# Optimization experiments

Hardware: AMD Instinct MI355X
Metric: run time of the kernel (lower is better)

## Reference

```python
import jax, jax.numpy as jnp
import numpy as np

C, H, OUT = 64, 128, 64          # in_channels, hidden_dim, out_channels
N, E = 20000, 640000             # nodes, edges
LN_EPS = 1e-5


def layer_norm(x, g, b):
    mu = jnp.mean(x, axis=-1, keepdims=True)
    var = jnp.var(x, axis=-1, keepdims=True)
    return (x - mu) * jax.lax.rsqrt(var + LN_EPS) * g + b


def setup_inputs() -> dict:
    key = jax.random.key(0)
    ks = jax.random.split(key, 12)
    F = 2 * C + 5  # edge MLP input dim = 133

    def w(k, shape, fan_in):
        return jax.random.normal(k, shape, jnp.float32) / np.float32(np.sqrt(fan_in))

    return {
        "x": jax.random.normal(ks[0], (N, C), jnp.float32),
        "pos": jax.random.normal(ks[1], (N, 2), jnp.float32),
        "vel": jax.random.normal(ks[2], (N, 2), jnp.float32),
        # phi_e: Linear(F,H) -> LN -> Softplus -> Linear(H,H) -> Softplus -> Linear(H,H)
        "We1": w(ks[3], (F, H), F), "be1": jnp.zeros((H,), jnp.float32),
        "ge1": jnp.ones((H,), jnp.float32), "bte1": jnp.zeros((H,), jnp.float32),
        "We2": w(ks[4], (H, H), H), "be2": jnp.zeros((H,), jnp.float32),
        "We3": w(ks[5], (H, H), H), "be3": jnp.zeros((H,), jnp.float32),
        # phi_v: Linear(F,H) -> LN -> Softplus -> Linear(H,1)
        "Wv1": w(ks[6], (F, H), F), "bv1": jnp.zeros((H,), jnp.float32),
        "gv1": jnp.ones((H,), jnp.float32), "btv1": jnp.zeros((H,), jnp.float32),
        "Wv2": w(ks[7], (H, 1), H), "bv2": jnp.zeros((1,), jnp.float32),
        # phi_h: Linear(C+H+1,H) -> LN -> Softplus -> Linear(H,OUT)
        "Wh1": w(ks[8], (C + H + 1, H), C + H + 1), "bh1": jnp.zeros((H,), jnp.float32),
        "gh1": jnp.ones((H,), jnp.float32), "bth1": jnp.zeros((H,), jnp.float32),
        "Wh2": w(ks[9], (H, OUT), H), "bh2": jnp.zeros((OUT,), jnp.float32),
        "edge_index": jax.random.randint(ks[10], (2, E), 0, N, dtype=jnp.int64)
        if jax.config.jax_enable_x64 else jax.random.randint(ks[10], (2, E), 0, N, dtype=jnp.int32),
    }


def reference(x, pos, vel,
              We1, be1, ge1, bte1, We2, be2, We3, be3,
              Wv1, bv1, gv1, btv1, Wv2, bv2,
              Wh1, bh1, gh1, bth1, Wh2, bh2,
              edge_index):
    src = edge_index[0]  # j (source / x_j)
    dst = edge_index[1]  # i (target / x_i, aggregation index)

    # per-edge geometric features (gather)
    rel_pos = pos[src] - pos[dst]                                   # [E,2]
    rel_vel = vel[src] - vel[dst]                                   # [E,2]
    dist_sq = jnp.sum(rel_pos ** 2, axis=-1, keepdims=True)         # [E,1]
    dot_vr = jnp.sum(rel_vel * rel_pos, axis=-1, keepdims=True)     # [E,1]
    r2_inv = jnp.minimum(1.0 / (dist_sq + 0.05), 20.0)
    r6_inv = jnp.minimum(r2_inv ** 3, 400.0)
    r12_inv = jnp.minimum(r6_inv ** 2, 160000.0)

    tmp = jnp.concatenate([x[dst], x[src], dist_sq, dot_vr,
                           r2_inv, r6_inv, r12_inv], axis=1)        # [E, 2C+5]

    # phi_e (edge MLP)
    h = jax.nn.softplus(layer_norm(tmp @ We1 + be1, ge1, bte1))
    h = jax.nn.softplus(h @ We2 + be2)
    m_h_e = h @ We3 + be3                                           # [E,H]

    # phi_v (scalar weight on rel_pos -> equivariant vector message)
    v = jax.nn.softplus(layer_norm(tmp @ Wv1 + bv1, gv1, btv1))
    v_w = v @ Wv2 + bv2                                             # [E,1]
    m_v_e = v_w * rel_pos                                           # [E,2]

    # scatter-mean aggregation to target nodes
    n_nodes = x.shape[0]
    ones = jnp.ones((src.shape[0], 1), x.dtype)
    cnt = jax.ops.segment_sum(ones, dst, num_segments=n_nodes)
    denom = jnp.maximum(cnt, 1.0)
    m_h = jax.ops.segment_sum(m_h_e, dst, num_segments=n_nodes) / denom   # [N,H]
    m_v = jax.ops.segment_sum(m_v_e, dst, num_segments=n_nodes) / denom   # [N,2]

    m_v_norm = jnp.sqrt(jnp.sum((m_v + 1e-8) ** 2, axis=-1, keepdims=True))  # [N,1]

    # phi_h (node update MLP); shortcut is Identity since C == OUT
    hin = jnp.concatenate([x, m_h, m_v_norm], axis=-1)              # [N, C+H+1]
    hu = jax.nn.softplus(layer_norm(hin @ Wh1 + bh1, gh1, bth1))
    h_update = hu @ Wh2 + bh2                                       # [N,OUT]
    return x + h_update
```

## Files before the change

### kernel.cpp

```cpp
#include <hip/hip_runtime.h>
#include <stdint.h>

#define NCH    64
#define HID    128
#define OUTC   64
#define NNODE  20000
#define NEDGE  640000
#define FDIM   133
#define TE     32
#define TN     32
#define LN_EPS 1e-5f
#define KP1    160
#define KP2    128
#define KN1    224
#define CAGS   130
#define NEBLK  (NEDGE / TE)
#define XSTR   (NEBLK / 8)

typedef __attribute__((ext_vector_type(8))) short bf16x8;
typedef __attribute__((ext_vector_type(4))) float f32x4;

__device__ __forceinline__ unsigned short f2bf(float f) {
    union { float f; unsigned int i; } v; v.f = f;
    unsigned int b = v.i;
    return (unsigned short)((b + 0x7FFFu + ((b >> 16) & 1u)) >> 16);
}
#if defined(__has_builtin)
#if __has_builtin(__builtin_amdgcn_cvt_pk_bf16_f32)
#define HAVE_PK_BF16 1
#endif
#endif
__device__ __forceinline__ unsigned int f2bf_pk(float a, float b) {
#ifdef HAVE_PK_BF16
    auto r = __builtin_amdgcn_cvt_pk_bf16_f32(a, b);
    return __builtin_bit_cast(unsigned int, r);
#else
    return (unsigned int)f2bf(a) | ((unsigned int)f2bf(b) << 16);
#endif
}
__device__ __forceinline__ float bfu2f(unsigned short u) {
    union { unsigned int i; float f; } v; v.i = ((unsigned int)u) << 16; return v.f;
}
__device__ __forceinline__ float sp(float xv) {
    return fmaxf(xv, 0.f) + __logf(1.0f + __expf(-fabsf(xv)));
}
__device__ __forceinline__ void atomAddF(float* p, float v) {
    __hip_atomic_fetch_add(p, v, __ATOMIC_RELAXED, __HIP_MEMORY_SCOPE_AGENT);
}
template<int PAT> __device__ __forceinline__ float shx(float v) {
    int i = __builtin_amdgcn_ds_swizzle(__builtin_bit_cast(int, v), PAT);
    return __builtin_bit_cast(float, i);
}
#define RED16(v) { v += shx<0x041F>(v); v += shx<0x081F>(v); v += shx<0x101F>(v); v += shx<0x201F>(v); }

__device__ __forceinline__ int fragOff(int ks, int mt, int lanepos) {
    return ((ks * 2 + mt) * 64 + lanepos) * 8;
}

#define WT_WE1 0
#define WT_WV1 (128 * KP1)
#define WT_WE2 (2 * 128 * KP1)
#define WT_WE3 (2 * 128 * KP1 + 128 * KP2)
#define WT_WH1 (2 * 128 * KP1 + 2 * 128 * KP2)
#define WT_WH2 (WT_WH1 + 128 * KN1)
#define WT_TOTAL (WT_WH2 + 64 * KP2)
#define PKP_N  1153

__global__ __launch_bounds__(256)
void eg_prep(const float* __restrict__ We1, const float* __restrict__ Wv1,
             const float* __restrict__ We2, const float* __restrict__ We3,
             const float* __restrict__ Wh1, const float* __restrict__ Wh2,
             const float* __restrict__ be1, const float* __restrict__ bv1,
             const float* __restrict__ ge1, const float* __restrict__ bte1,
             const float* __restrict__ gv1, const float* __restrict__ btv1,
             const float* __restrict__ Wv2, const float* __restrict__ be2,
             const float* __restrict__ be3, const float* __restrict__ bv2,
             const int* __restrict__ ei,
             short* __restrict__ wt, float* __restrict__ pkp,
             int* __restrict__ deg)
{
    int idx = blockIdx.x * 256 + threadIdx.x;
    if (idx < WT_TOTAL) {
        short v;
        if (idx < WT_WV1) {
            int n = idx / KP1, k = idx % KP1;
            v = (k < FDIM) ? (short)f2bf(We1[(size_t)k * HID + n]) : (short)0;
        } else if (idx < WT_WE2) {
            int r = idx - WT_WV1; int n = r / KP1, k = r % KP1;
            v = (k < FDIM) ? (short)f2bf(Wv1[(size_t)k * HID + n]) : (short)0;
        } else if (idx < WT_WE3) {
            int r = idx - WT_WE2; int n = r / KP2, k = r % KP2;
            v = (short)f2bf(We2[(size_t)k * HID + n]);
        } else if (idx < WT_WH1) {
            int r = idx - WT_WE3; int n = r / KP2, k = r % KP2;
            v = (short)f2bf(We3[(size_t)k * HID + n]);
        } else if (idx < WT_WH2) {
            int r = idx - WT_WH1; int n = r / KN1, k = r % KN1;
            v = (k < 193) ? (short)f2bf(Wh1[(size_t)k * HID + n]) : (short)0;
        } else {
            int r = idx - WT_WH2; int n = r / KP2, k = r % KP2;
            v = (short)f2bf(Wh2[(size_t)k * OUTC + n]);
        }
        wt[idx] = v;
    }
    if (idx < PKP_N) {
        float pv;
        int k = idx >> 7, c = idx & 127;
        switch (k) {
            case 0: pv = be1[c]; break;
            case 1: pv = bv1[c]; break;
            case 2: pv = ge1[c]; break;
            case 3: pv = bte1[c]; break;
            case 4: pv = gv1[c]; break;
            case 5: pv = btv1[c]; break;
            case 6: pv = Wv2[c]; break;
            case 7: pv = be2[c]; break;
            case 8: pv = be3[c]; break;
            default: pv = bv2[0]; break;
        }
        pkp[idx] = pv;
    }
    if (idx < NEDGE)
        __hip_atomic_fetch_add(&deg[ei[NEDGE + idx]], 1, __ATOMIC_RELAXED, __HIP_MEMORY_SCOPE_AGENT);
}

__global__ __launch_bounds__(1024)
void eg_scan(const int* __restrict__ deg, int* __restrict__ cur)
{
    __shared__ int part[1024];
    const int tid = threadIdx.x;
    const int chunk = (NNODE + 1023) / 1024;
    const int base = tid * chunk;
    const int lim = min(base + chunk, NNODE);
    int s = 0;
    for (int j = base; j < lim; ++j) s += deg[j];
    part[tid] = s;
    __syncthreads();
    for (int off = 1; off < 1024; off <<= 1) {
        int v = (tid >= off) ? part[tid - off] : 0;
        __syncthreads();
        part[tid] += v;
        __syncthreads();
    }
    int run = (tid > 0) ? part[tid - 1] : 0;
    for (int j = base; j < lim; ++j) { cur[j] = run; run += deg[j]; }
}

__global__ __launch_bounds__(256)
void eg_scatter(const int* __restrict__ ei, int* __restrict__ cur,
                int* __restrict__ perm)
{
    int i = blockIdx.x * 256 + threadIdx.x;
    if (i < NEDGE) {
        int d = ei[NEDGE + i];
        int p = __hip_atomic_fetch_add(&cur[d], 1, __ATOMIC_RELAXED, __HIP_MEMORY_SCOPE_AGENT);
        perm[p] = i;
    }
}

__global__ __launch_bounds__(256, 7)
void eg_edge(const float* __restrict__ x, const float* __restrict__ pos,
             const float* __restrict__ vel,
             const float* __restrict__ pkp,
             const short* __restrict__ wt,
             const int* __restrict__ ei, const int* __restrict__ perm,
             float* __restrict__ mh, float* __restrict__ mv)
{
    __shared__ __align__(16) short frag_s[5 * 2 * 64 * 8];
    __shared__ __align__(4) unsigned short cagg_s[TE * CAGS];
    __shared__ float psum_s[512];
    __shared__ float mu_s[64], rs_s[64];
    __shared__ int   dst_s[TE], src_s[TE];
    __shared__ float rel_s[TE * 2], vw_s[TE];

    const int tid  = threadIdx.x;
    const int lane = tid & 63;
    const int wid  = tid >> 6;
    const int lr   = lane & 15;
    const int quad = lane >> 4;
    const int n0w  = wid * 32;
    const int bid  = (blockIdx.x & 7) * XSTR + (blockIdx.x >> 3);
    const int e_base = bid * TE;

    const short* We1T = wt + WT_WE1;
    const short* Wv1T = wt + WT_WV1;
    const short* We2T = wt + WT_WE2;
    const short* We3T = wt + WT_WE3;

    float geo[5];
    if (tid < TE) {
        int gi = perm[e_base + tid];
        int eS = ei[gi];
        int eD = ei[NEDGE + gi];
        src_s[tid] = eS; dst_s[tid] = eD;
        float rx = pos[2 * eS]     - pos[2 * eD];
        float ry = pos[2 * eS + 1] - pos[2 * eD + 1];
        float vx = vel[2 * eS]     - vel[2 * eD];
        float vy = vel[2 * eS + 1] - vel[2 * eD + 1];
        float dsq = rx * rx + ry * ry;
        float dvr = vx * rx + vy * ry;
        float r2  = fminf(1.0f / (dsq + 0.05f), 20.0f);
        float r6  = fminf(r2 * r2 * r2, 400.0f);
        float r12 = fminf(r6 * r6, 160000.0f);
        geo[0] = dsq; geo[1] = dvr; geo[2] = r2; geo[3] = r6; geo[4] = r12;
        rel_s[2 * tid] = rx; rel_s[2 * tid + 1] = ry;
    }
    if (tid < 128) {
        int4 z = {0, 0, 0, 0};
        *(int4*)&frag_s[4 * 2 * 64 * 8 + tid * 8] = z;
    }
    __syncthreads();

    if (tid < TE) {
        int off = fragOff(4, tid >> 4, (tid & 15));
        #pragma unroll
        for (int j = 0; j < 5; ++j) frag_s[off + j] = (short)f2bf(geo[j]);
    }
    {
        const int e = tid & 31, slot = tid >> 5;
        const int d = dst_s[e], s = src_s[e];
        #pragma unroll
        for (int h = 0; h < 2; ++h) {
            int o = slot + h * 8;
            int node = h ? s : d;
            int c0 = (o & 7) * 8;
            const float4 a0 = *(const float4*)&x[(size_t)node * NCH + c0];
            const float4 a1 = *(const float4*)&x[(size_t)node * NCH + c0 + 4];
            uint4 pk;
            pk.x = f2bf_pk(a0.x, a0.y); pk.y = f2bf_pk(a0.z, a0.w);
            pk.z = f2bf_pk(a1.x, a1.y); pk.w = f2bf_pk(a1.z, a1.w);
            int ks = o >> 2, kq = o & 3;
            *(uint4*)&frag_s[fragOff(ks, e >> 4, kq * 16 + (e & 15))] = pk;
        }
    }
    __syncthreads();

    const int ncol0 = n0w + lr;
    const int ncol1 = n0w + 16 + lr;
    const float* p0 = pkp + ncol0;
    const float* p1 = pkp + ncol1;

    f32x4 zero4 = {0.f, 0.f, 0.f, 0.f};
    f32x4 accE[2][2], accV[2][2];
    #pragma unroll
    for (int mt = 0; mt < 2; ++mt)
        #pragma unroll
        for (int nt = 0; nt < 2; ++nt) { accE[mt][nt] = zero4; accV[mt][nt] = zero4; }
    {
        const short* pa = &frag_s[lane * 8];
        const short* pwE0 = We1T + ncol0 * KP1 + quad * 8;
        const short* pwE1 = We1T + ncol1 * KP1 + quad * 8;
        const short* pwV0 = Wv1T + ncol0 * KP1 + quad * 8;
        const short* pwV1 = Wv1T + ncol1 * KP1 + quad * 8;
        #pragma unroll
        for (int ks = 0; ks < 5; ++ks) {
            bf16x8 af0 = *(const bf16x8*)&pa[ks * 1024];
            bf16x8 af1 = *(const bf16x8*)&pa[ks * 1024 + 512];
            bf16x8 bwE0 = *(const bf16x8*)&pwE0[ks * 32];
            bf16x8 bwE1 = *(const bf16x8*)&pwE1[ks * 32];
            bf16x8 bwV0 = *(const bf16x8*)&pwV0[ks * 32];
            bf16x8 bwV1 = *(const bf16x8*)&pwV1[ks * 32];
            accE[0][0] = __builtin_amdgcn_mfma_f32_16x16x32_bf16(af0, bwE0, accE[0][0], 0, 0, 0);
            accE[1][0] = __builtin_amdgcn_mfma_f32_16x16x32_bf16(af1, bwE0, accE[1][0], 0, 0, 0);
            accE[0][1] = __builtin_amdgcn_mfma_f32_16x16x32_bf16(af0, bwE1, accE[0][1], 0, 0, 0);
            accE[1][1] = __builtin_amdgcn_mfma_f32_16x16x32_bf16(af1, bwE1, accE[1][1], 0, 0, 0);
            accV[0][0] = __builtin_amdgcn_mfma_f32_16x16x32_bf16(af0, bwV0, accV[0][0], 0, 0, 0);
            accV[1][0] = __builtin_amdgcn_mfma_f32_16x16x32_bf16(af1, bwV0, accV[1][0], 0, 0, 0);
            accV[0][1] = __builtin_amdgcn_mfma_f32_16x16x32_bf16(af0, bwV1, accV[0][1], 0, 0, 0);
            accV[1][1] = __builtin_amdgcn_mfma_f32_16x16x32_bf16(af1, bwV1, accV[1][1], 0, 0, 0);
        }
    }
    {
        float be0 = p0[0], be_1 = p1[0];
        float bv0 = p0[128], bv_1 = p1[128];
        #pragma unroll
        for (int mt = 0; mt < 2; ++mt)
            #pragma unroll
            for (int r = 0; r < 4; ++r) {
                accE[mt][0][r] += be0; accE[mt][1][r] += be_1;
                accV[mt][0][r] += bv0; accV[mt][1][r] += bv_1;
            }
    }

    #pragma unroll
    for (int mt = 0; mt < 2; ++mt)
        #pragma unroll
        for (int r = 0; r < 4; ++r) {
            float se = accE[mt][0][r] + accE[mt][1][r];
            float qe = accE[mt][0][r] * accE[mt][0][r] + accE[mt][1][r] * accE[mt][1][r];
            float sv = accV[mt][0][r] + accV[mt][1][r];
            float qv = accV[mt][0][r] * accV[mt][0][r] + accV[mt][1][r] * accV[mt][1][r];
            RED16(se); RED16(qe); RED16(sv); RED16(qv);
            if (lr == 0) {
                int row = mt * 16 + quad * 4 + r;
                psum_s[      row * 4 + wid] = se;
                psum_s[128 + row * 4 + wid] = qe;
                psum_s[256 + row * 4 + wid] = sv;
                psum_s[384 + row * 4 + wid] = qv;
            }
        }
    __syncthreads();
    if (tid < 64) {
        int p = tid >> 5, row = tid & 31;
        float s = 0.f, q = 0.f;
        #pragma unroll
        for (int w = 0; w < 4; ++w) {
            s += psum_s[p * 256 +       row * 4 + w];
            q += psum_s[p * 256 + 128 + row * 4 + w];
        }
        float mu = s * (1.0f / HID);
        float var = q * (1.0f / HID) - mu * mu;
        mu_s[p * 32 + row] = mu;
        rs_s[p * 32 + row] = rsqrtf(var + LN_EPS);
    }
    __syncthreads();

    {
        float gE0 = p0[256], gE1 = p1[256];
        float tE0 = p0[384], tE1 = p1[384];
        float gV0 = p0[512], gV1 = p1[512];
        float tV0 = p0[640], tV1 = p1[640];
        float w20 = p0[768], w21 = p1[768];
        int ks0 = ncol0 >> 5, kq0 = (ncol0 & 31) >> 3, j0 = ncol0 & 7;
        int ks1 = ncol1 >> 5, kq1 = (ncol1 & 31) >> 3, j1 = ncol1 & 7;
        short* bp0 = &frag_s[(ks0 * 128 + kq0 * 16 + quad * 4) * 8 + j0];
        short* bp1 = &frag_s[(ks1 * 128 + kq1 * 16 + quad * 4) * 8 + j1];
        #pragma unroll
        for (int mt = 0; mt < 2; ++mt)
            #pragma unroll
            for (int r = 0; r < 4; ++r) {
                int rlow = quad * 4 + r, row = mt * 16 + rlow;
                float mu = mu_s[row], rsv = rs_s[row];
                float muV = mu_s[32 + row], rsV = rs_s[32 + row];
                float h0 = sp((accE[mt][0][r] - mu) * rsv * gE0 + tE0);
                float h1 = sp((accE[mt][1][r] - mu) * rsv * gE1 + tE1);
                unsigned int ph = f2bf_pk(h0, h1);
                bp0[mt * 512 + r * 8] = (short)(ph & 0xFFFFu);
                bp1[mt * 512 + r * 8] = (short)(ph >> 16);
                float v0 = sp((accV[mt][0][r] - muV) * rsV * gV0 + tV0);
                float v1 = sp((accV[mt][1][r] - muV) * rsV * gV1 + tV1);
                float vp = v0 * w20 + v1 * w21;
                RED16(vp);
                if (lr == 0) psum_s[row * 4 + wid] = vp;
            }
    }
    __syncthreads();
    if (tid < TE) {
        float s = 0.f;
        #pragma unroll
        for (int w = 0; w < 4; ++w) s += psum_s[tid * 4 + w];
        vw_s[tid] = s + pkp[1152];
    }

    {
        f32x4 acc2[2][2];
        #pragma unroll
        for (int mt = 0; mt < 2; ++mt)
            #pragma unroll
            for (int nt = 0; nt < 2; ++nt) acc2[mt][nt] = zero4;
        {
            const short* pa = &frag_s[lane * 8];
            const short* pw0 = We2T + ncol0 * KP2 + quad * 8;
            const short* pw1 = We2T + ncol1 * KP2 + quad * 8;
            #pragma unroll
            for (int ks = 0; ks < 4; ++ks) {
                bf16x8 af0 = *(const bf16x8*)&pa[ks * 1024];
                bf16x8 af1 = *(const bf16x8*)&pa[ks * 1024 + 512];
                bf16x8 bw0 = *(const bf16x8*)&pw0[ks * 32];
                bf16x8 bw1 = *(const bf16x8*)&pw1[ks * 32];
                acc2[0][0] = __builtin_amdgcn_mfma_f32_16x16x32_bf16(af0, bw0, acc2[0][0], 0, 0, 0);
                acc2[1][0] = __builtin_amdgcn_mfma_f32_16x16x32_bf16(af1, bw0, acc2[1][0], 0, 0, 0);
                acc2[0][1] = __builtin_amdgcn_mfma_f32_16x16x32_bf16(af0, bw1, acc2[0][1], 0, 0, 0);
                acc2[1][1] = __builtin_amdgcn_mfma_f32_16x16x32_bf16(af1, bw1, acc2[1][1], 0, 0, 0);
            }
        }
        __syncthreads();
        float b2a = p0[896], b2b = p1[896];
        int ksA = ncol0 >> 5, kqA = (ncol0 & 31) >> 3, jA = ncol0 & 7;
        int ksB = ncol1 >> 5, kqB = (ncol1 & 31) >> 3, jB = ncol1 & 7;
        short* bpA = &frag_s[(ksA * 128 + kqA * 16 + quad * 4) * 8 + jA];
        short* bpB = &frag_s[(ksB * 128 + kqB * 16 + quad * 4) * 8 + jB];
        #pragma unroll
        for (int mt = 0; mt < 2; ++mt)
            #pragma unroll
            for (int r = 0; r < 4; ++r) {
                bpA[mt * 512 + r * 8] = (short)f2bf(sp(acc2[mt][0][r] + b2a));
                bpB[mt * 512 + r * 8] = (short)f2bf(sp(acc2[mt][1][r] + b2b));
            }
    }
    __syncthreads();

    {
        f32x4 acc3[2][2];
        #pragma unroll
        for (int mt = 0; mt < 2; ++mt)
            #pragma unroll
            for (int nt = 0; nt < 2; ++nt) acc3[mt][nt] = zero4;
        {
            const short* pa = &frag_s[lane * 8];
            const short* pw0 = We3T + ncol0 * KP2 + quad * 8;
            const short* pw1 = We3T + ncol1 * KP2 + quad * 8;
            #pragma unroll
            for (int ks = 0; ks < 4; ++ks) {
                bf16x8 af0 = *(const bf16x8*)&pa[ks * 1024];
                bf16x8 af1 = *(const bf16x8*)&pa[ks * 1024 + 512];
                bf16x8 bw0 = *(const bf16x8*)&pw0[ks * 32];
                bf16x8 bw1 = *(const bf16x8*)&pw1[ks * 32];
                acc3[0][0] = __builtin_amdgcn_mfma_f32_16x16x32_bf16(af0, bw0, acc3[0][0], 0, 0, 0);
                acc3[1][0] = __builtin_amdgcn_mfma_f32_16x16x32_bf16(af1, bw0, acc3[1][0], 0, 0, 0);
                acc3[0][1] = __builtin_amdgcn_mfma_f32_16x16x32_bf16(af0, bw1, acc3[0][1], 0, 0, 0);
                acc3[1][1] = __builtin_amdgcn_mfma_f32_16x16x32_bf16(af1, bw1, acc3[1][1], 0, 0, 0);
            }
        }
        float b3a = p0[1024], b3b = p1[1024];
        unsigned short* bpA = &cagg_s[(quad * 4) * CAGS + ncol0];
        unsigned short* bpB = &cagg_s[(quad * 4) * CAGS + ncol1];
        #pragma unroll
        for (int mt = 0; mt < 2; ++mt)
            #pragma unroll
            for (int r = 0; r < 4; ++r) {
                bpA[(mt * 16 + r) * CAGS] = f2bf(acc3[mt][0][r] + b3a);
                bpB[(mt * 16 + r) * CAGS] = f2bf(acc3[mt][1][r] + b3b);
            }
    }
    __syncthreads();

    {
        const int c = tid & 127, h = tid >> 7;
        const unsigned short* cp = &cagg_s[(h * 16) * CAGS + c];
        const int m0 = h * 16;
        float run = bfu2f(cp[0]);
        int curd = dst_s[m0];
        #pragma unroll
        for (int m = 1; m < 16; ++m) {
            int d = dst_s[m0 + m];
            float v = bfu2f(cp[m * CAGS]);
            if (d == curd) run += v;
            else { atomAddF(&mh[(size_t)curd * HID + c], run); curd = d; run = v; }
        }
        atomAddF(&mh[(size_t)curd * HID + c], run);
    }
    if (tid < 2) {
        const int c = tid;
        float run = vw_s[0] * rel_s[c];
        int curd = dst_s[0];
        for (int m = 1; m < TE; ++m) {
            int d = dst_s[m];
            float v = vw_s[m] * rel_s[2 * m + c];
            if (d == curd) run += v;
            else { atomAddF(&mv[2 * curd + c], run); curd = d; run = v; }
        }
        atomAddF(&mv[2 * curd + c], run);
    }
}

__global__ __launch_bounds__(256, 7)
void eg_node(const float* __restrict__ x,
             const float* __restrict__ bh1, const float* __restrict__ gh1,
             const float* __restrict__ bth1, const float* __restrict__ bh2,
             const float* __restrict__ mh, const float* __restrict__ mv,
             const int* __restrict__ deg, const short* __restrict__ wt,
             float* __restrict__ out)
{
    __shared__ __align__(16) short frag_s[7 * 2 * 64 * 8];
    __shared__ float psum_s[256];
    __shared__ float mu_s[32], rs_s[32];
    __shared__ float rden_s[TN], norm_s[TN];

    const int tid  = threadIdx.x;
    const int lane = tid & 63;
    const int wid  = tid >> 6;
    const int lr   = lane & 15;
    const int quad = lane >> 4;
    const int n0w  = wid * 32;
    const int n_base = blockIdx.x * TN;

    const short* Wh1T = wt + WT_WH1;
    const short* Wh2T = wt + WT_WH2;

    if (tid < TN) {
        int n = n_base + tid;
        float den = fmaxf((float)deg[n], 1.0f);
        float rd = 1.0f / den;
        float ax = mv[2 * n] * rd + 1e-8f;
        float ay = mv[2 * n + 1] * rd + 1e-8f;
        rden_s[tid] = rd;
        norm_s[tid] = sqrtf(ax * ax + ay * ay);
    }
    if (tid < 128) {
        int4 z = {0, 0, 0, 0};
        *(int4*)&frag_s[6 * 2 * 64 * 8 + tid * 8] = z;
    }
    __syncthreads();

    {
        const int e = tid & 31, slot = tid >> 5;
        const int n = n_base + e;
        {
            int c0 = slot * 8;
            const float4 a0 = *(const float4*)&x[(size_t)n * NCH + c0];
            const float4 a1 = *(const float4*)&x[(size_t)n * NCH + c0 + 4];
            uint4 pk;
            pk.x = f2bf_pk(a0.x, a0.y); pk.y = f2bf_pk(a0.z, a0.w);
            pk.z = f2bf_pk(a1.x, a1.y); pk.w = f2bf_pk(a1.z, a1.w);
            int ks = slot >> 2, kq = slot & 3;
            *(uint4*)&frag_s[fragOff(ks, e >> 4, kq * 16 + (e & 15))] = pk;
        }
        float rd = rden_s[e];
        #pragma unroll
        for (int h = 0; h < 2; ++h) {
            int o = 8 + slot + h * 8;
            int k0 = (o - 8) * 8;
            const float4 a0 = *(const float4*)&mh[(size_t)n * HID + k0];
            const float4 a1 = *(const float4*)&mh[(size_t)n * HID + k0 + 4];
            uint4 pk;
            pk.x = f2bf_pk(a0.x * rd, a0.y * rd); pk.y = f2bf_pk(a0.z * rd, a0.w * rd);
            pk.z = f2bf_pk(a1.x * rd, a1.y * rd); pk.w = f2bf_pk(a1.z * rd, a1.w * rd);
            int ks = o >> 2, kq = o & 3;
            *(uint4*)&frag_s[fragOff(ks, e >> 4, kq * 16 + (e & 15))] = pk;
        }
    }
    if (tid < TN) {
        frag_s[fragOff(6, tid >> 4, (tid & 15))] = (short)f2bf(norm_s[tid]);
    }
    __syncthreads();

    const int ncol0 = n0w + lr;
    const int ncol1 = n0w + 16 + lr;

    f32x4 zero4 = {0.f, 0.f, 0.f, 0.f};
    f32x4 acc1[2][2];
    #pragma unroll
    for (int mt = 0; mt < 2; ++mt)
        #pragma unroll
        for (int nt = 0; nt < 2; ++nt) acc1[mt][nt] = zero4;
    {
        const short* pa = &frag_s[lane * 8];
        const short* pw0 = Wh1T + ncol0 * KN1 + quad * 8;
        const short* pw1 = Wh1T + ncol1 * KN1 + quad * 8;
        #pragma unroll
        for (int ks = 0; ks < 7; ++ks) {
            bf16x8 af0 = *(const bf16x8*)&pa[ks * 1024];
            bf16x8 af1 = *(const bf16x8*)&pa[ks * 1024 + 512];
            bf16x8 bw0 = *(const bf16x8*)&pw0[ks * 32];
            bf16x8 bw1 = *(const bf16x8*)&pw1[ks * 32];
            acc1[0][0] = __builtin_amdgcn_mfma_f32_16x16x32_bf16(af0, bw0, acc1[0][0], 0, 0, 0);
            acc1[1][0] = __builtin_amdgcn_mfma_f32_16x16x32_bf16(af1, bw0, acc1[1][0], 0, 0, 0);
            acc1[0][1] = __builtin_amdgcn_mfma_f32_16x16x32_bf16(af0, bw1, acc1[0][1], 0, 0, 0);
            acc1[1][1] = __builtin_amdgcn_mfma_f32_16x16x32_bf16(af1, bw1, acc1[1][1], 0, 0, 0);
        }
    }
    {
        float b0 = bh1[ncol0], b1 = bh1[ncol1];
        #pragma unroll
        for (int mt = 0; mt < 2; ++mt)
            #pragma unroll
            for (int r = 0; r < 4; ++r) { acc1[mt][0][r] += b0; acc1[mt][1][r] += b1; }
    }

    #pragma unroll
    for (int mt = 0; mt < 2; ++mt)
        #pragma unroll
        for (int r = 0; r < 4; ++r) {
            float s = acc1[mt][0][r] + acc1[mt][1][r];
            float q = acc1[mt][0][r] * acc1[mt][0][r] + acc1[mt][1][r] * acc1[mt][1][r];
            RED16(s); RED16(q);
            if (lr == 0) {
                int row = mt * 16 + quad * 4 + r;
                psum_s[row * 4 + wid]       = s;
                psum_s[128 + row * 4 + wid] = q;
            }
        }
    __syncthreads();
    if (tid < 32) {
        float s = 0.f, q = 0.f;
        #pragma unroll
        for (int w = 0; w < 4; ++w) {
            s += psum_s[tid * 4 + w];
            q += psum_s[128 + tid * 4 + w];
        }
        float mu = s * (1.0f / HID);
        float var = q * (1.0f / HID) - mu * mu;
        mu_s[tid] = mu;
        rs_s[tid] = rsqrtf(var + LN_EPS);
    }
    __syncthreads();

    {
        float g0 = gh1[ncol0], g1 = gh1[ncol1];
        float t0 = bth1[ncol0], t1 = bth1[ncol1];
        int ks0 = ncol0 >> 5, kq0 = (ncol0 & 31) >> 3, j0 = ncol0 & 7;
        int ks1 = ncol1 >> 5, kq1 = (ncol1 & 31) >> 3, j1 = ncol1 & 7;
        short* bp0 = &frag_s[(ks0 * 128 + kq0 * 16 + quad * 4) * 8 + j0];
        short* bp1 = &frag_s[(ks1 * 128 + kq1 * 16 + quad * 4) * 8 + j1];
        #pragma unroll
        for (int mt = 0; mt < 2; ++mt)
            #pragma unroll
            for (int r = 0; r < 4; ++r) {
                int row = mt * 16 + quad * 4 + r;
                float mu = mu_s[row], rsv = rs_s[row];
                float h0 = sp((acc1[mt][0][r] - mu) * rsv * g0 + t0);
                float h1 = sp((acc1[mt][1][r] - mu) * rsv * g1 + t1);
                unsigned int ph = f2bf_pk(h0, h1);
                bp0[mt * 512 + r * 8] = (short)(ph & 0xFFFFu);
                bp1[mt * 512 + r * 8] = (short)(ph >> 16);
            }
    }
    __syncthreads();

    {
        const int col = wid * 16 + lr;
        f32x4 acc2[2] = { zero4, zero4 };
        const short* pa = &frag_s[lane * 8];
        const short* pw = Wh2T + col * KP2 + quad * 8;
        #pragma unroll
        for (int ks = 0; ks < 4; ++ks) {
            bf16x8 af0 = *(const bf16x8*)&pa[ks * 1024];
            bf16x8 af1 = *(const bf16x8*)&pa[ks * 1024 + 512];
            bf16x8 bw = *(const bf16x8*)&pw[ks * 32];
            acc2[0] = __builtin_amdgcn_mfma_f32_16x16x32_bf16(af0, bw, acc2[0], 0, 0, 0);
            acc2[1] = __builtin_amdgcn_mfma_f32_16x16x32_bf16(af1, bw, acc2[1], 0, 0, 0);
        }
        float bo = bh2[col];
        #pragma unroll
        for (int mt = 0; mt < 2; ++mt)
            #pragma unroll
            for (int r = 0; r < 4; ++r) {
                int m = mt * 16 + quad * 4 + r;
                size_t idx = (size_t)(n_base + m) * OUTC + col;
                out[idx] = x[(size_t)(n_base + m) * NCH + col] + acc2[mt][r] + bo;
            }
    }
}

extern "C" void kernel_launch(void* const* d_in, const int* in_sizes, int n_in,
                              void* d_out, int out_size, void* d_ws, size_t ws_size,
                              hipStream_t stream)
{
    const float* x    = (const float*)d_in[0];
    const float* pos  = (const float*)d_in[1];
    const float* vel  = (const float*)d_in[2];
    const float* We1  = (const float*)d_in[3];
    const float* be1  = (const float*)d_in[4];
    const float* ge1  = (const float*)d_in[5];
    const float* bte1 = (const float*)d_in[6];
    const float* We2  = (const float*)d_in[7];
    const float* be2  = (const float*)d_in[8];
    const float* We3  = (const float*)d_in[9];
    const float* be3  = (const float*)d_in[10];
    const float* Wv1  = (const float*)d_in[11];
    const float* bv1  = (const float*)d_in[12];
    const float* gv1  = (const float*)d_in[13];
    const float* btv1 = (const float*)d_in[14];
    const float* Wv2  = (const float*)d_in[15];
    const float* bv2  = (const float*)d_in[16];
    const float* Wh1  = (const float*)d_in[17];
    const float* bh1  = (const float*)d_in[18];
    const float* gh1  = (const float*)d_in[19];
    const float* bth1 = (const float*)d_in[20];
    const float* Wh2  = (const float*)d_in[21];
    const float* bh2  = (const float*)d_in[22];
    const int*   ei   = (const int*)d_in[23];

    float* mh   = (float*)d_ws;
    float* mv   = mh + (size_t)NNODE * HID;
    int*   deg  = (int*)(mv + NNODE * 2);
    int*   cur  = deg + NNODE;
    int*   perm = cur + NNODE;
    float* pkp  = (float*)(perm + NEDGE);
    short* wt   = (short*)(pkp + 1280);

    size_t zbytes = ((size_t)NNODE * HID + NNODE * 2 + NNODE) * sizeof(float);
    hipMemsetAsync(d_ws, 0, zbytes, stream);

    eg_prep<<<dim3(NEDGE / 256), dim3(256), 0, stream>>>(
        We1, Wv1, We2, We3, Wh1, Wh2,
        be1, bv1, ge1, bte1, gv1, btv1, Wv2, be2, be3, bv2,
        ei, wt, pkp, deg);
    eg_scan<<<dim3(1), dim3(1024), 0, stream>>>(deg, cur);
    eg_scatter<<<dim3(NEDGE / 256), dim3(256), 0, stream>>>(ei, cur, perm);

    eg_edge<<<dim3(NEBLK), dim3(256), 0, stream>>>(
        x, pos, vel, pkp, wt, ei, perm, mh, mv);

    eg_node<<<dim3(NNODE / TN), dim3(256), 0, stream>>>(
        x, bh1, gh1, bth1, bh2, mh, mv, deg, wt, (float*)d_out);
}
```

Before: 517.7 us.

## Alias edge output staging onto fragment LDS, fold zeroing into prep, pack bf16

The edge kernel's separate cagg_s staging buffer is removed and the layer-3 output is staged in the frag_s region after an extra barrier. This cuts LDS use so the launch bound can rise from 7 to 8 blocks per CU. Zeroing of the mh/mv accumulators moves out of a large memset and into the prep kernel's threads, leaving only a small memset for deg. bf16 conversions are done as packed pairs. The cost is one more __syncthreads per edge block, plus reliance on the prep grid size exactly covering the zeroed range.

```diff
diff --git a/kernel.cpp b/kernel.cpp
--- a/kernel.cpp
+++ b/kernel.cpp
@@ -77,9 +77,14 @@
              const float* __restrict__ be3, const float* __restrict__ bv2,
              const int* __restrict__ ei,
              short* __restrict__ wt, float* __restrict__ pkp,
-             int* __restrict__ deg)
+             int* __restrict__ deg, float* __restrict__ mhz)
 {
     int idx = blockIdx.x * 256 + threadIdx.x;
+    {
+        float4 z = {0.f, 0.f, 0.f, 0.f};
+        ((float4*)mhz)[idx] = z;
+        if (idx < 10000) ((float4*)mhz)[640000 + idx] = z;
+    }
     if (idx < WT_TOTAL) {
         short v;
         if (idx < WT_WV1) {
@@ -158,7 +163,7 @@
     }
 }
 
-__global__ __launch_bounds__(256, 7)
+__global__ __launch_bounds__(256, 8)
 void eg_edge(const float* __restrict__ x, const float* __restrict__ pos,
              const float* __restrict__ vel,
              const float* __restrict__ pkp,
@@ -167,7 +172,6 @@
              float* __restrict__ mh, float* __restrict__ mv)
 {
     __shared__ __align__(16) short frag_s[5 * 2 * 64 * 8];
-    __shared__ __align__(4) unsigned short cagg_s[TE * CAGS];
     __shared__ float psum_s[512];
     __shared__ float mu_s[64], rs_s[64];
     __shared__ int   dst_s[TE], src_s[TE];
@@ -381,12 +385,20 @@
         short* bpA = &frag_s[(ksA * 128 + kqA * 16 + quad * 4) * 8 + jA];
         short* bpB = &frag_s[(ksB * 128 + kqB * 16 + quad * 4) * 8 + jB];
         #pragma unroll
-        for (int mt = 0; mt < 2; ++mt)
-            #pragma unroll
-            for (int r = 0; r < 4; ++r) {
-                bpA[mt * 512 + r * 8] = (short)f2bf(sp(acc2[mt][0][r] + b2a));
-                bpB[mt * 512 + r * 8] = (short)f2bf(sp(acc2[mt][1][r] + b2b));
-            }
+        for (int mt = 0; mt < 2; ++mt) {
+            unsigned int uA0 = f2bf_pk(sp(acc2[mt][0][0] + b2a), sp(acc2[mt][0][1] + b2a));
+            unsigned int uA1 = f2bf_pk(sp(acc2[mt][0][2] + b2a), sp(acc2[mt][0][3] + b2a));
+            unsigned int uB0 = f2bf_pk(sp(acc2[mt][1][0] + b2b), sp(acc2[mt][1][1] + b2b));
+            unsigned int uB1 = f2bf_pk(sp(acc2[mt][1][2] + b2b), sp(acc2[mt][1][3] + b2b));
+            bpA[mt * 512 +  0] = (short)(uA0 & 0xFFFFu);
+            bpA[mt * 512 +  8] = (short)(uA0 >> 16);
+            bpA[mt * 512 + 16] = (short)(uA1 & 0xFFFFu);
+            bpA[mt * 512 + 24] = (short)(uA1 >> 16);
+            bpB[mt * 512 +  0] = (short)(uB0 & 0xFFFFu);
+            bpB[mt * 512 +  8] = (short)(uB0 >> 16);
+            bpB[mt * 512 + 16] = (short)(uB1 & 0xFFFFu);
+            bpB[mt * 512 + 24] = (short)(uB1 >> 16);
+        }
     }
     __syncthreads();
 
@@ -412,20 +424,31 @@
                 acc3[1][1] = __builtin_amdgcn_mfma_f32_16x16x32_bf16(af1, bw1, acc3[1][1], 0, 0, 0);
             }
         }
+        __syncthreads();
+        unsigned short* cagg_s = (unsigned short*)frag_s;
         float b3a = p0[1024], b3b = p1[1024];
         unsigned short* bpA = &cagg_s[(quad * 4) * CAGS + ncol0];
         unsigned short* bpB = &cagg_s[(quad * 4) * CAGS + ncol1];
         #pragma unroll
-        for (int mt = 0; mt < 2; ++mt)
-            #pragma unroll
-            for (int r = 0; r < 4; ++r) {
-                bpA[(mt * 16 + r) * CAGS] = f2bf(acc3[mt][0][r] + b3a);
-                bpB[(mt * 16 + r) * CAGS] = f2bf(acc3[mt][1][r] + b3b);
-            }
-    }
-    __syncthreads();
-
-    {
+        for (int mt = 0; mt < 2; ++mt) {
+            unsigned int uA0 = f2bf_pk(acc3[mt][0][0] + b3a, acc3[mt][0][1] + b3a);
+            unsigned int uA1 = f2bf_pk(acc3[mt][0][2] + b3a, acc3[mt][0][3] + b3a);
+            unsigned int uB0 = f2bf_pk(acc3[mt][1][0] + b3b, acc3[mt][1][1] + b3b);
+            unsigned int uB1 = f2bf_pk(acc3[mt][1][2] + b3b, acc3[mt][1][3] + b3b);
+            bpA[(mt * 16 + 0) * CAGS] = (unsigned short)(uA0 & 0xFFFFu);
+            bpA[(mt * 16 + 1) * CAGS] = (unsigned short)(uA0 >> 16);
+            bpA[(mt * 16 + 2) * CAGS] = (unsigned short)(uA1 & 0xFFFFu);
+            bpA[(mt * 16 + 3) * CAGS] = (unsigned short)(uA1 >> 16);
+            bpB[(mt * 16 + 0) * CAGS] = (unsigned short)(uB0 & 0xFFFFu);
+            bpB[(mt * 16 + 1) * CAGS] = (unsigned short)(uB0 >> 16);
+            bpB[(mt * 16 + 2) * CAGS] = (unsigned short)(uB1 & 0xFFFFu);
+            bpB[(mt * 16 + 3) * CAGS] = (unsigned short)(uB1 >> 16);
+        }
+    }
+    __syncthreads();
+
+    {
+        const unsigned short* cagg_s = (const unsigned short*)frag_s;
         const int c = tid & 127, h = tid >> 7;
         const unsigned short* cp = &cagg_s[(h * 16) * CAGS + c];
         const int m0 = h * 16;
@@ -670,13 +693,12 @@
     float* pkp  = (float*)(perm + NEDGE);
     short* wt   = (short*)(pkp + 1280);
 
-    size_t zbytes = ((size_t)NNODE * HID + NNODE * 2 + NNODE) * sizeof(float);
-    hipMemsetAsync(d_ws, 0, zbytes, stream);
+    hipMemsetAsync(deg, 0, NNODE * sizeof(int), stream);
 
     eg_prep<<<dim3(NEDGE / 256), dim3(256), 0, stream>>>(
         We1, Wv1, We2, We3, Wh1, Wh2,
         be1, bv1, ge1, bte1, gv1, btv1, Wv2, be2, be3, bv2,
-        ei, wt, pkp, deg);
+        ei, wt, pkp, deg, mh);
     eg_scan<<<dim3(1), dim3(1024), 0, stream>>>(deg, cur);
     eg_scatter<<<dim3(NEDGE / 256), dim3(256), 0, stream>>>(ei, cur, perm);
 
```

Result: slower. 575.4 us (+11.1%).
